# Optimization experiments

Hardware: AMD Instinct MI355X
Metric: run time of the kernel (lower is better)

## Reference

```python
import jax, jax.numpy as jnp
import numpy as np

NB_HEAD = 16
SIZE_PER_HEAD = 64


def setup_inputs() -> dict:
    key = jax.random.key(0)
    k1, k2 = jax.random.split(key)
    x = jax.random.normal(k1, (2, 2048, 1024), dtype=jnp.float32)
    kernel = jax.random.normal(k2, (3, 1024, NB_HEAD * SIZE_PER_HEAD), dtype=jnp.float32) * 0.02
    return {"x": x, "kernel": kernel}


def reference(x, kernel):
    B, S, D = x.shape
    H, dh = NB_HEAD, SIZE_PER_HEAD
    # QKV projections: [B,S,D] @ [D, H*dh] -> [B,S,H,dh] -> [B,H,S,dh]
    def proj(w):
        return jnp.einsum('bsd,de->bse', x, w).reshape(B, S, H, dh).transpose(0, 2, 1, 3)
    Q = proj(kernel[0])
    Ks = proj(kernel[1])
    V = proj(kernel[2])
    scores = jnp.einsum('bhqd,bhkd->bhqk', Q, Ks) / jnp.sqrt(jnp.float32(dh))
    attn = jax.nn.softmax(scores, axis=-1)
    z = jnp.einsum('bhqk,bhkd->bhqd', attn, V)  # [B,H,S,dh]
    return z.transpose(0, 2, 1, 3).reshape(B, S, H * dh)
```

## Files before the change

### kernel.cpp

```cpp
#include <hip/hip_runtime.h>
#include <hip/hip_bf16.h>

#define HB 16
#define DH 64
#define SQ 2048
#define BB 2

using f32x4 = __attribute__((ext_vector_type(4))) float;
using f32x16 = __attribute__((ext_vector_type(16))) float;
using s16x8 = __attribute__((ext_vector_type(8))) short;

__device__ __forceinline__ unsigned bfr(float f) {
    union { float f; unsigned u; } v; v.f = f;
    return (v.u + 0x7fffu + ((v.u >> 16) & 1u)) >> 16;
}
__device__ __forceinline__ unsigned pk2(float a, float b) { return bfr(a) | (bfr(b) << 16); }
__device__ __forceinline__ short f2bf(float f) { return (short)bfr(f); }

__device__ __forceinline__ int swz64(int r, int c) {
    return r * 64 + ((((c >> 3) ^ (r & 7)) & 7) << 3) + (c & 7);
}
__device__ __forceinline__ int swz32(int r, int c) {
    return r * 32 + ((((c >> 3) ^ ((r >> 1) & 3)) & 3) << 3) + (c & 7);
}

__device__ __forceinline__ void gll16(const short* g, short* l) {
    __builtin_amdgcn_global_load_lds(
        (const __attribute__((address_space(1))) unsigned int*)(uintptr_t)g,
        (__attribute__((address_space(3))) unsigned int*)(uintptr_t)l, 16, 0, 0);
}

__device__ __forceinline__ int swzT(int n, int k) {
    return n * 64 + ((((k >> 3) ^ ((n >> 2) & 7)) & 7) << 3) + (k & 7);
}
__global__ __launch_bounds__(256) void cvt_all(
    const float* __restrict__ x, const float* __restrict__ w,
    short* __restrict__ xb, short* __restrict__ wt)
{
    __shared__ short T[64 * 64];
    int bid = blockIdx.x;
    int t = threadIdx.x;
    if (bid < 2048) {
        int i = (bid * 256 + t) * 8;
        float4 v0 = *(const float4*)&x[i];
        float4 v1 = *(const float4*)&x[i + 4];
        uint4 u;
        u.x = pk2(v0.x, v0.y); u.y = pk2(v0.z, v0.w);
        u.z = pk2(v1.x, v1.y); u.w = pk2(v1.z, v1.w);
        *(uint4*)&xb[i] = u;
        return;
    }
    bid -= 2048;
    int nt = bid & 15, kt = (bid >> 4) & 15, p = bid >> 8;
    const float* wp = w + p * 1048576 + (kt * 64) * 1024 + nt * 64;
    short* wtp = wt + p * 1048576 + (nt * 64) * 1024 + kt * 64;
#pragma unroll
    for (int ps = 0; ps < 4; ps++) {
        int idx = ps * 1024 + t * 4;
        int r = idx >> 6, c = idx & 63;
        float4 v = *(const float4*)&wp[r * 1024 + c];
        T[swzT(c + 0, r)] = f2bf(v.x);
        T[swzT(c + 1, r)] = f2bf(v.y);
        T[swzT(c + 2, r)] = f2bf(v.z);
        T[swzT(c + 3, r)] = f2bf(v.w);
    }
    __syncthreads();
#pragma unroll
    for (int ps = 0; ps < 2; ps++) {
        int idx = ps * 2048 + t * 8;
        int n = idx >> 6, kc = idx & 63;
        s16x8 vv = *(const s16x8*)&T[swzT(n, kc)];
        *(s16x8*)&wtp[n * 1024 + kc] = vv;
    }
}

__global__ __launch_bounds__(512, 1) void qkv_gemm(
    const short* __restrict__ xb, const short* __restrict__ wt, short* __restrict__ ws)
{
    __shared__ short Xs[3][128 * 32];
    __shared__ short Ns[3][384 * 32];
    const int tid = threadIdx.x;
    const int wv = tid >> 6, ln = tid & 63;
    const int bid = blockIdx.x;
    const int swz = (bid & 7) * 32 + (bid >> 3);
    const int m0 = (swz & 31) * 128;
    const int n0 = (swz >> 5) * 128;

    const int wm = (wv >> 2) * 64, wn = (wv & 3) * 96;
    const int lr = ln & 15, lk = (ln >> 4) * 8;
    const int srow = tid >> 2;
    const int csw = (((tid & 3) ^ ((tid >> 3) & 3)) & 3) * 8;

    f32x4 acc[4][6] = {};

#define GSTAGE(k0_, bf_) do {                                                   \
        gll16(&xb[(m0 + srow) * 1024 + (k0_) + csw], &Xs[bf_][wv * 512]);       \
        _Pragma("unroll")                                                       \
        for (int p_ = 0; p_ < 3; p_++)                                          \
            gll16(&wt[p_ * 1048576 + (n0 + srow) * 1024 + (k0_) + csw],         \
                  &Ns[bf_][p_ * 4096 + wv * 512]);                              \
    } while (0)

#define GCOMP(bf_) do {                                                         \
        s16x8 af[4], bg[6];                                                     \
        _Pragma("unroll")                                                       \
        for (int i = 0; i < 4; i++)                                             \
            af[i] = *(const s16x8*)&Xs[bf_][swz32(wm + i * 16 + lr, lk)];       \
        _Pragma("unroll")                                                       \
        for (int j = 0; j < 6; j++)                                             \
            bg[j] = *(const s16x8*)&Ns[bf_][swz32(wn + j * 16 + lr, lk)];       \
        __builtin_amdgcn_s_setprio(1);                                          \
        _Pragma("unroll")                                                       \
        for (int i = 0; i < 4; i++)                                             \
            _Pragma("unroll")                                                   \
            for (int j = 0; j < 6; j++)                                         \
                acc[i][j] = __builtin_amdgcn_mfma_f32_16x16x32_bf16(af[i], bg[j], acc[i][j], 0, 0, 0); \
        __builtin_amdgcn_s_setprio(0);                                          \
    } while (0)

    GSTAGE(0, 0);
    GSTAGE(32, 1);
    int cur = 0;
    for (int t = 0; t < 31; t++) {
        asm volatile("s_waitcnt vmcnt(4)\n\ts_barrier" ::: "memory");
        int pre = cur + 2; if (pre >= 3) pre -= 3;
        if (t < 30) GSTAGE((t + 2) * 32, pre);
        GCOMP(cur);
        cur = (cur == 2) ? 0 : cur + 1;
    }
    asm volatile("s_waitcnt vmcnt(0)\n\ts_barrier" ::: "memory");
    GCOMP(cur);

    short* qws = ws;
    short* kws = ws + BB * HB * SQ * DH;
    short* vtw = ws + 2 * BB * HB * SQ * DH;
#pragma unroll
    for (int i = 0; i < 4; i++) {
#pragma unroll
        for (int r = 0; r < 4; r++) {
            int row = m0 + wm + i * 16 + (ln >> 4) * 4 + r;
            int b = row >> 11, s = row & 2047;
#pragma unroll
            for (int j = 0; j < 6; j++) {
                int c = wn + j * 16 + (ln & 15);
                int p = c >> 7;
                int gcol = n0 + (c & 127);
                int h = gcol >> 6, dhi = gcol & 63;
                float v = acc[i][j][r];
                if (p == 0)      qws[((b * HB + h) * SQ + s) * DH + dhi] = f2bf(v * 0.1803368801f);
                else if (p == 1) kws[((b * HB + h) * SQ + s) * DH + dhi] = f2bf(v);
                else             vtw[((b * HB + h) * DH + dhi) * SQ + s] = f2bf(v);
            }
        }
    }
#undef GSTAGE
#undef GCOMP
}

__global__ __launch_bounds__(512) void attn(
    const short* __restrict__ qws, const short* __restrict__ kws,
    const short* __restrict__ vtw, float* __restrict__ out)
{
    __shared__ __align__(16) short smem[24576];
    __shared__ float Lx[4][32];
    const int tid = threadIdx.x, wv = tid >> 6, ln = tid & 63;
    const int ws_ = wv & 3, g = wv >> 2;
    const int bid = blockIdx.x;
    const int swz = (bid & 7) * 64 + (bid >> 3);
    const int qt = swz & 15, bh = swz >> 4;
    const short* Q = qws + bh * SQ * DH;
    const short* K = kws + bh * SQ * DH;
    const short* VT = vtw + bh * DH * SQ;
    const int lq = ln & 31, lg = ln >> 5;
    const int q0w = qt * 128 + ws_ * 32;
    const int kvbase = g * 1024;

    const int klo = (ws_ * 8 + (ln >> 3)) * DH + (((ln & 7) ^ ((ln >> 3) & 7)) & 7) * 8;
    const int vr = ln >> 2;
    const int vlo = (ws_ * 16 + vr) * SQ + (((ln & 3) ^ ((vr >> 1) & 3)) & 3) * 8;

    s16x8 qf[4];
#pragma unroll
    for (int ks = 0; ks < 4; ks++)
        qf[ks] = *(const s16x8*)&Q[(q0w + lq) * DH + ks * 16 + lg * 8];

    f32x16 o0 = {}, o1 = {};
    float l = 0.f;

#define STAGE(t, bf_) do {                                          \
        short* Kd = smem + g * 12288 + (bf_) * 4096;                \
        const short* Kt = K + (kvbase + (t) * 32) * DH;             \
        const short* Vt = VT + kvbase + (t) * 32;                   \
        gll16(Kt + klo, Kd + ws_ * 512);                            \
        gll16(Vt + vlo, Kd + 2048 + ws_ * 512);                     \
    } while (0)

#define QKT(bf_, S_) do {                                                      \
        const short* Kr = smem + g * 12288 + (bf_) * 4096;                     \
        __builtin_amdgcn_s_setprio(1);                                         \
        _Pragma("unroll")                                                      \
        for (int ks = 0; ks < 4; ks++) {                                       \
            s16x8 ka = *(const s16x8*)&Kr[swz64(lq, ks * 16 + lg * 8)];        \
            S_ = __builtin_amdgcn_mfma_f32_32x32x16_bf16(ka, qf[ks], S_, 0, 0, 0); \
        }                                                                      \
        __builtin_amdgcn_s_setprio(0);                                         \
    } while (0)

#define SMPV(bf_, S_) do {                                                     \
        const short* Vr = smem + g * 12288 + (bf_) * 4096 + 2048;              \
        float p[16];                                                           \
        _Pragma("unroll")                                                      \
        for (int i = 0; i < 16; i++) p[i] = __builtin_amdgcn_exp2f(S_[i]);     \
        float a0 = 0.f, a1 = 0.f, a2 = 0.f, a3 = 0.f;                          \
        _Pragma("unroll")                                                      \
        for (int i = 0; i < 16; i += 4) {                                      \
            a0 += p[i]; a1 += p[i + 1]; a2 += p[i + 2]; a3 += p[i + 3];        \
        }                                                                      \
        l += (a0 + a1) + (a2 + a3);                                            \
        unsigned u[8];                                                         \
        _Pragma("unroll")                                                      \
        for (int qd = 0; qd < 4; qd++) {                                       \
            asm("v_cvt_pk_bf16_f32 %0, %1, %2" : "=v"(u[qd * 2]) : "v"(p[qd * 4 + 0]), "v"(p[qd * 4 + 1])); \
            asm("v_cvt_pk_bf16_f32 %0, %1, %2" : "=v"(u[qd * 2 + 1]) : "v"(p[qd * 4 + 2]), "v"(p[qd * 4 + 3])); \
        }                                                                      \
        _Pragma("unroll")                                                      \
        for (int m2 = 0; m2 < 2; m2++)                                         \
            _Pragma("unroll")                                                  \
            for (int j = 0; j < 2; j++)                                        \
                asm("v_permlane32_swap_b32 %0, %1"                             \
                    : "+v"(u[(2 * m2) * 2 + j]), "+v"(u[(2 * m2 + 1) * 2 + j])); \
        __builtin_amdgcn_s_setprio(1);                                         \
        _Pragma("unroll")                                                      \
        for (int ks = 0; ks < 2; ks++) {                                       \
            union { unsigned w[4]; s16x8 v; } pa;                              \
            pa.w[0] = u[4 * ks + 0];                                           \
            pa.w[1] = u[4 * ks + 1];                                           \
            pa.w[2] = u[4 * ks + 2];                                           \
            pa.w[3] = u[4 * ks + 3];                                           \
            s16x8 vb0 = *(const s16x8*)&Vr[swz32(lq, ks * 16 + lg * 8)];       \
            s16x8 vb1 = *(const s16x8*)&Vr[swz32(32 + lq, ks * 16 + lg * 8)];  \
            o0 = __builtin_amdgcn_mfma_f32_32x32x16_bf16(pa.v, vb0, o0, 0, 0, 0); \
            o1 = __builtin_amdgcn_mfma_f32_32x32x16_bf16(pa.v, vb1, o1, 0, 0, 0); \
        }                                                                      \
        __builtin_amdgcn_s_setprio(0);                                         \
    } while (0)

    STAGE(0, 0);
    STAGE(1, 1);
    __syncthreads();
    f32x16 sA = {}, sB = {};
    QKT(0, sA);
#pragma unroll
    for (int t = 0; t < 32; t++) {
        if (t < 30) STAGE(t + 2, (t + 2) % 3);
        if (t < 31) {
            if (t & 1) QKT((t + 1) % 3, sA);
            else       QKT((t + 1) % 3, sB);
        }
        if (t & 1) SMPV(t % 3, sB);
        else       SMPV(t % 3, sA);
        if (t & 1) sB = (f32x16){};
        else       sA = (f32x16){};
        __syncthreads();
    }

    float lt = l + __shfl_xor(l, 32);
    float* Lf = (float*)smem;
    if (g == 1) {
#pragma unroll
        for (int r = 0; r < 16; r++) {
            Lf[ws_ * 1024 + r * 64 + ln] = o0[r];
            Lf[4096 + ws_ * 1024 + r * 64 + ln] = o1[r];
        }
        if (lg == 0) Lx[ws_][lq] = lt;
    }
    __syncthreads();
    if (g == 0) {
        float inv = 1.0f / (lt + Lx[ws_][lq]);
        const int b = bh >> 4, h = bh & 15;
#pragma unroll
        for (int r = 0; r < 16; r++) {
            int qrow = (r & 3) + 8 * (r >> 2) + 4 * lg;
            float iv = __shfl(inv, qrow);
            float* op = out + ((long)(b * SQ + q0w + qrow)) * 1024 + h * 64 + lq;
            op[0]  = (o0[r] + Lf[ws_ * 1024 + r * 64 + ln]) * iv;
            op[32] = (o1[r] + Lf[4096 + ws_ * 1024 + r * 64 + ln]) * iv;
        }
    }
#undef STAGE
#undef QKT
#undef SMPV
}

extern "C" void kernel_launch(void* const* d_in, const int* in_sizes, int n_in,
                              void* d_out, int out_size, void* d_ws, size_t ws_size,
                              hipStream_t stream) {
    const float* x = (const float*)d_in[0];
    const float* w = (const float*)d_in[1];
    short* ws = (short*)d_ws;
    short* xbf = (short*)d_out;
    short* wtb = (short*)d_out + 4194304;
    cvt_all<<<2816, 256, 0, stream>>>(x, w, xbf, wtb);
    qkv_gemm<<<256, 512, 0, stream>>>(xbf, wtb, ws);
    attn<<<512, 512, 0, stream>>>(ws, ws + BB * HB * SQ * DH,
                                  ws + 2 * BB * HB * SQ * DH, (float*)d_out);
}
```

Measured before the change: 89.71 us.

## Split attention KV range across four wave groups with 1024-thread blocks

Doubles the attention block to 1024 threads so four wave groups each process a quarter of the key/value sequence instead of two halves. The three-buffer software pipeline with interleaved QK^T and softmax-PV is replaced by a simple double-buffered loop that computes both per tile. The cross-group reduction of partial outputs and row sums now goes through shared memory in two passes to fit LDS. This is meant to raise parallelism and shorten each wave's serial loop. In exchange it loses the QK/softmax overlap, adds reduction traffic and syncs, and puts register pressure on the launch bound of 1024 threads.

```diff
diff --git a/kernel.cpp b/kernel.cpp
--- a/kernel.cpp
+++ b/kernel.cpp
@@ -157,12 +157,12 @@
 #undef GCOMP
 }
 
-__global__ __launch_bounds__(512) void attn(
+__global__ __launch_bounds__(1024, 8) void attn(
     const short* __restrict__ qws, const short* __restrict__ kws,
     const short* __restrict__ vtw, float* __restrict__ out)
 {
-    __shared__ __align__(16) short smem[24576];
-    __shared__ float Lx[4][32];
+    __shared__ __align__(16) short smem[32768];
+    __shared__ float Lx[3][4][32];
     const int tid = threadIdx.x, wv = tid >> 6, ln = tid & 63;
     const int ws_ = wv & 3, g = wv >> 2;
     const int bid = blockIdx.x;
@@ -173,7 +173,7 @@
     const short* VT = vtw + bh * DH * SQ;
     const int lq = ln & 31, lg = ln >> 5;
     const int q0w = qt * 128 + ws_ * 32;
-    const int kvbase = g * 1024;
+    const int kvbase = g * 512;
 
     const int klo = (ws_ * 8 + (ln >> 3)) * DH + (((ln & 7) ^ ((ln >> 3) & 7)) & 7) * 8;
     const int vr = ln >> 2;
@@ -188,29 +188,27 @@
     float l = 0.f;
 
 #define STAGE(t, bf_) do {                                          \
-        short* Kd = smem + g * 12288 + (bf_) * 4096;                \
+        short* Kd = smem + g * 8192 + (bf_) * 4096;                 \
         const short* Kt = K + (kvbase + (t) * 32) * DH;             \
         const short* Vt = VT + kvbase + (t) * 32;                   \
         gll16(Kt + klo, Kd + ws_ * 512);                            \
         gll16(Vt + vlo, Kd + 2048 + ws_ * 512);                     \
     } while (0)
 
-#define QKT(bf_, S_) do {                                                      \
-        const short* Kr = smem + g * 12288 + (bf_) * 4096;                     \
+#define COMPUTE(bf_) do {                                                      \
+        const short* Kr = smem + g * 8192 + (bf_) * 4096;                      \
+        const short* Vr = Kr + 2048;                                           \
+        f32x16 s = {};                                                         \
         __builtin_amdgcn_s_setprio(1);                                         \
         _Pragma("unroll")                                                      \
         for (int ks = 0; ks < 4; ks++) {                                       \
             s16x8 ka = *(const s16x8*)&Kr[swz64(lq, ks * 16 + lg * 8)];        \
-            S_ = __builtin_amdgcn_mfma_f32_32x32x16_bf16(ka, qf[ks], S_, 0, 0, 0); \
+            s = __builtin_amdgcn_mfma_f32_32x32x16_bf16(ka, qf[ks], s, 0, 0, 0); \
         }                                                                      \
         __builtin_amdgcn_s_setprio(0);                                         \
-    } while (0)
-
-#define SMPV(bf_, S_) do {                                                     \
-        const short* Vr = smem + g * 12288 + (bf_) * 4096 + 2048;              \
         float p[16];                                                           \
         _Pragma("unroll")                                                      \
-        for (int i = 0; i < 16; i++) p[i] = __builtin_amdgcn_exp2f(S_[i]);     \
+        for (int i = 0; i < 16; i++) p[i] = __builtin_amdgcn_exp2f(s[i]);      \
         float a0 = 0.f, a1 = 0.f, a2 = 0.f, a3 = 0.f;                          \
         _Pragma("unroll")                                                      \
         for (int i = 0; i < 16; i += 4) {                                      \
@@ -246,50 +244,55 @@
     } while (0)
 
     STAGE(0, 0);
-    STAGE(1, 1);
-    __syncthreads();
-    f32x16 sA = {}, sB = {};
-    QKT(0, sA);
-#pragma unroll
-    for (int t = 0; t < 32; t++) {
-        if (t < 30) STAGE(t + 2, (t + 2) % 3);
-        if (t < 31) {
-            if (t & 1) QKT((t + 1) % 3, sA);
-            else       QKT((t + 1) % 3, sB);
-        }
-        if (t & 1) SMPV(t % 3, sB);
-        else       SMPV(t % 3, sA);
-        if (t & 1) sB = (f32x16){};
-        else       sA = (f32x16){};
+    __syncthreads();
+    for (int t = 0; t < 16; t++) {
+        int cur = t & 1;
+        if (t < 15) STAGE(t + 1, cur ^ 1);
+        COMPUTE(cur);
         __syncthreads();
     }
 
     float lt = l + __shfl_xor(l, 32);
     float* Lf = (float*)smem;
-    if (g == 1) {
+    if (g > 0) {
+        int base = ((g - 1) * 4 + ws_) * 1024;
+#pragma unroll
+        for (int r = 0; r < 16; r++) Lf[base + r * 64 + ln] = o0[r];
+        if (lg == 0) Lx[g - 1][ws_][lq] = lt;
+    }
+    __syncthreads();
+    float inv = 0.f;
+    if (g == 0) {
+        inv = 1.0f / (lt + Lx[0][ws_][lq] + Lx[1][ws_][lq] + Lx[2][ws_][lq]);
+#pragma unroll
+        for (int r = 0; r < 16; r++)
+            o0[r] += Lf[ws_ * 1024 + r * 64 + ln]
+                   + Lf[(4 + ws_) * 1024 + r * 64 + ln]
+                   + Lf[(8 + ws_) * 1024 + r * 64 + ln];
+    }
+    __syncthreads();
+    if (g > 0) {
+        int base = ((g - 1) * 4 + ws_) * 1024;
+#pragma unroll
+        for (int r = 0; r < 16; r++) Lf[base + r * 64 + ln] = o1[r];
+    }
+    __syncthreads();
+    if (g == 0) {
+        const int b = bh >> 4, h = bh & 15;
 #pragma unroll
         for (int r = 0; r < 16; r++) {
-            Lf[ws_ * 1024 + r * 64 + ln] = o0[r];
-            Lf[4096 + ws_ * 1024 + r * 64 + ln] = o1[r];
-        }
-        if (lg == 0) Lx[ws_][lq] = lt;
-    }
-    __syncthreads();
-    if (g == 0) {
-        float inv = 1.0f / (lt + Lx[ws_][lq]);
-        const int b = bh >> 4, h = bh & 15;
-#pragma unroll
-        for (int r = 0; r < 16; r++) {
+            float v1 = o1[r] + Lf[ws_ * 1024 + r * 64 + ln]
+                             + Lf[(4 + ws_) * 1024 + r * 64 + ln]
+                             + Lf[(8 + ws_) * 1024 + r * 64 + ln];
             int qrow = (r & 3) + 8 * (r >> 2) + 4 * lg;
             float iv = __shfl(inv, qrow);
             float* op = out + ((long)(b * SQ + q0w + qrow)) * 1024 + h * 64 + lq;
-            op[0]  = (o0[r] + Lf[ws_ * 1024 + r * 64 + ln]) * iv;
-            op[32] = (o1[r] + Lf[4096 + ws_ * 1024 + r * 64 + ln]) * iv;
+            op[0]  = o0[r] * iv;
+            op[32] = v1 * iv;
         }
     }
 #undef STAGE
-#undef QKT
-#undef SMPV
+#undef COMPUTE
 }
 
 extern "C" void kernel_launch(void* const* d_in, const int* in_sizes, int n_in,
@@ -302,6 +305,6 @@
     short* wtb = (short*)d_out + 4194304;
     cvt_all<<<2816, 256, 0, stream>>>(x, w, xbf, wtb);
     qkv_gemm<<<256, 512, 0, stream>>>(xbf, wtb, ws);
-    attn<<<512, 512, 0, stream>>>(ws, ws + BB * HB * SQ * DH,
-                                  ws + 2 * BB * HB * SQ * DH, (float*)d_out);
-}
+    attn<<<512, 1024, 0, stream>>>(ws, ws + BB * HB * SQ * DH,
+                                   ws + 2 * BB * HB * SQ * DH, (float*)d_out);
+}
```

After: 182.2 us. +103.1%, slower.
